# Optimization experiments

Measured on AMD Instinct MI355X. Metric: run time of the kernel, lower is better.

The kernel has to match this reference:

```python
import jax, jax.numpy as jnp
import numpy as np

# Dims: B=batch, C=n_car, N=n_node, E=embed_dim, H=n_heads
B, C, N, E = 64, 8, 512, 512
H = 8
CLIP = 10.0


def setup_inputs() -> dict:
    key = jax.random.key(0)
    ks = jax.random.split(key, 12)
    s = 1.0 / np.sqrt(E)
    mask = jax.random.bernoulli(ks[10], 0.3, (B, C, 1, N))
    mask = mask.at[..., 0].set(False)  # ensure at least one unmasked node per (b,c)
    return {
        "node_embeddings": jax.random.normal(ks[0], (B, N, E), jnp.float32),
        "graph_embedding": jax.random.normal(ks[1], (B, E), jnp.float32),
        "step_context": jax.random.normal(ks[2], (B, C, 1, E + 2), jnp.float32),
        "mask": mask,
        "Wk1": jax.random.normal(ks[3], (E, E), jnp.float32) * s,
        "Wv": jax.random.normal(ks[4], (E, E), jnp.float32) * s,
        "Wk2": jax.random.normal(ks[5], (E, E), jnp.float32) * s,
        "Wq_fixed": jax.random.normal(ks[6], (E, E), jnp.float32) * s,
        "Wout": jax.random.normal(ks[7], (E, E), jnp.float32) * s,
        "Wq_step": jax.random.normal(ks[8], (E, E + 2), jnp.float32) * s,
        "v": jax.random.uniform(ks[9], (E,), jnp.float32, -s, s),
    }


def reference(node_embeddings, graph_embedding, step_context, mask,
              Wk1, Wv, Wk2, Wq_fixed, Wout, Wq_step, v):
    dh = E // H
    neg = jnp.asarray(-1e9, node_embeddings.dtype)

    # compute_static: projections (torch Linear: x @ W.T). K/V/Q_fixed are
    # broadcast over the car dim instead of materialized via .repeat (same math).
    Q_fixed = (graph_embedding @ Wq_fixed.T)[:, None, None, :]  # [B,1,1,E]
    K1 = node_embeddings @ Wk1.T                                 # [B,N,E]
    V = node_embeddings @ Wv.T                                   # [B,N,E]
    K2 = node_embeddings @ Wk2.T                                 # [B,N,E]

    # compute_dynamic
    Q_step = step_context @ Wq_step.T                            # [B,C,1,E]
    Q1 = Q_fixed + Q_step                                        # [B,C,1,E]

    # MHA (need_W=False): split heads, masked scaled dot-product, merge heads.
    qh = Q1.reshape(B, C, H, dh)                                 # q-len 1 squeezed
    kh = K1.reshape(B, N, H, dh)
    vh = V.reshape(B, N, H, dh)
    scores = jnp.einsum('bchd,bnhd->bchn', qh, kh) * (1.0 / np.sqrt(dh))
    m = mask[:, :, 0, :][:, :, None, :]                          # [B,C,1,N]
    scores = jnp.where(m, neg, scores)
    attn = jax.nn.softmax(scores, axis=-1)
    heads = jnp.einsum('bchn,bnhd->bchd', attn, vh).reshape(B, C, E)
    Q3 = heads @ Wout.T                                          # [B,C,E] (Q2.squeeze(2))

    # Pointer logits (SHA): u = tanh(Q_fixed+Q_step) @ v, repeated over E,
    # dotted with K2 => u_scalar * sum_e K2, then tanh-clipped and masked.
    u_scalar = jnp.einsum('bcqe,e->bcq', jnp.tanh(Q1), v)        # [B,C,1]
    k2sum = K2.sum(-1)                                           # [B,N]
    raw = u_scalar * k2sum[:, None, :]                           # [B,C,N]
    logits = CLIP * jnp.tanh(raw * (1.0 / np.sqrt(E)))
    logits = jnp.where(mask[:, :, 0, :], neg, logits)
    logits = logits.reshape(B, C * N)                            # view(batch, -1)
    return logits, Q3
```

## Files before the change

kernel.cpp:

```cpp
#include <hip/hip_runtime.h>


typedef _Float16 f16x8 __attribute__((ext_vector_type(8)));
typedef _Float16 f16x2 __attribute__((ext_vector_type(2)));
typedef float f32x4 __attribute__((ext_vector_type(4)));

__device__ __forceinline__ void async16(const void* g, void* l) {
  __builtin_amdgcn_global_load_lds(
      (const __attribute__((address_space(1))) unsigned int*)g,
      (__attribute__((address_space(3))) unsigned int*)l, 16, 0, 0);
}

__global__ __launch_bounds__(256) void prep_w(const float* __restrict__ Wk1,
                                              const float* __restrict__ Wv,
                                              const float* __restrict__ Wk2,
                                              _Float16* __restrict__ W1h,
                                              _Float16* __restrict__ W2h,
                                              float* __restrict__ colsum) {
  const int bid = blockIdx.x;
  if (bid < 16) {
    const int tx = threadIdx.x & 31, ty = threadIdx.x >> 5;
    const int col = bid * 32 + tx;
    float s = 0.f;
#pragma unroll 4
    for (int e = ty * 64; e < ty * 64 + 64; ++e) s += Wk2[e * 512 + col];
    __shared__ float red[8][32];
    red[ty][tx] = s;
    __syncthreads();
    if (ty == 0) {
      float t = 0.f;
#pragma unroll
      for (int g = 0; g < 8; ++g) t += red[g][tx];
      colsum[col] = t;
    }
  } else {
    const int cb = bid - 16;
    const float* src = (cb < 128) ? Wk1 : Wv;
    _Float16* dst = (cb < 128) ? W1h : W2h;
    const size_t off = (size_t)(cb & 127) * 2048 + threadIdx.x * 8;
    float4 a = *(const float4*)(src + off);
    float4 b = *(const float4*)(src + off + 4);
    union { _Float16 h[8]; uint4 u; } pk;
    pk.h[0] = (_Float16)a.x; pk.h[1] = (_Float16)a.y;
    pk.h[2] = (_Float16)a.z; pk.h[3] = (_Float16)a.w;
    pk.h[4] = (_Float16)b.x; pk.h[5] = (_Float16)b.y;
    pk.h[6] = (_Float16)b.z; pk.h[7] = (_Float16)b.w;
    *(uint4*)(dst + off) = pk.u;
  }
}

__global__ __launch_bounds__(256) void k2sum_kernel(const float* __restrict__ ne,
                                                    const float* __restrict__ colsum,
                                                    float* __restrict__ k2sum) {
  const int wave = threadIdx.x >> 6, lane = threadIdx.x & 63;
  const int row = blockIdx.x * 4 + wave;
  float s = 0.f;
#pragma unroll
  for (int i = 0; i < 8; ++i) {
    int k = i * 64 + lane;
    s += ne[(size_t)row * 512 + k] * colsum[k];
  }
#pragma unroll
  for (int off = 32; off; off >>= 1) s += __shfl_down(s, off, 64);
  if (lane == 0) k2sum[row] = s;
}

__global__ __launch_bounds__(256) void q1_mfma_kernel(
    const float* __restrict__ ge, const float* __restrict__ sc,
    const float* __restrict__ Wqf, const float* __restrict__ Wqs,
    float* __restrict__ Q1) {
  const int mb = blockIdx.x, nb = blockIdx.y, ks = blockIdx.z;
  const int tid = threadIdx.x;
  const int lane = tid & 63, wave = tid >> 6;
  const int wm = (wave >> 1) * 32, wn = (wave & 1) * 32;

  __shared__ __align__(16) _Float16 As[64][40];
  __shared__ __align__(16) _Float16 Ws[64][40];

  f32x4 acc[2][2] = {};
  const int qd = (lane >> 4) * 8, rr = lane & 15;

  for (int kt = 0; kt < 9; ++kt) {
    const int kb = ks * 288 + kt * 32;
#pragma unroll
    for (int f0 = 0; f0 < 2; ++f0) {
      int f = tid + f0 * 256;
      int r = f >> 3, c4 = (f & 7) * 4;
      int m = mb * 64 + r;
      int e = nb * 64 + r;
#pragma unroll
      for (int j = 0; j < 4; ++j) {
        int k = kb + c4 + j;
        float a = 0.f, w = 0.f;
        if (k < 512) {
          a = ge[(m >> 3) * 512 + k];
          w = Wqf[(size_t)e * 512 + k];
        } else if (k < 1026) {
          a = sc[(size_t)m * 514 + (k - 512)];
          w = Wqs[(size_t)e * 514 + (k - 512)];
        }
        As[r][c4 + j] = (_Float16)a;
        Ws[r][c4 + j] = (_Float16)w;
      }
    }
    __syncthreads();
    f16x8 af[2], bfr[2];
#pragma unroll
    for (int mi = 0; mi < 2; ++mi) af[mi] = *(const f16x8*)&As[wm + mi * 16 + rr][qd];
#pragma unroll
    for (int ni = 0; ni < 2; ++ni) bfr[ni] = *(const f16x8*)&Ws[wn + ni * 16 + rr][qd];
#pragma unroll
    for (int mi = 0; mi < 2; ++mi)
#pragma unroll
      for (int ni = 0; ni < 2; ++ni)
        acc[mi][ni] =
            __builtin_amdgcn_mfma_f32_16x16x32_f16(af[mi], bfr[ni], acc[mi][ni], 0, 0, 0);
    __syncthreads();
  }

  const int col = lane & 15, rq = (lane >> 4) * 4;
#pragma unroll
  for (int mi = 0; mi < 2; ++mi)
#pragma unroll
    for (int ni = 0; ni < 2; ++ni)
#pragma unroll
      for (int r = 0; r < 4; ++r) {
        int m = mb * 64 + wm + mi * 16 + rq + r;
        int e = nb * 64 + wn + ni * 16 + col;
        atomicAdd(&Q1[(size_t)m * 512 + e], acc[mi][ni][r]);
      }
}

__global__ __launch_bounds__(256, 2) void gemm_kv(
    const float* __restrict__ A, const _Float16* __restrict__ W1,
    const _Float16* __restrict__ W2, _Float16* __restrict__ K1,
    _Float16* __restrict__ V) {
  const int nb = blockIdx.x;
  const int mb = blockIdx.y;
  const int tid = threadIdx.x, lane = tid & 63, wave = tid >> 6;
  const int wm = (wave >> 1) * 64, wn = (wave & 1) * 64;
  const int row0 = mb * 128, col0 = nb * 128;

  __shared__ __align__(16) _Float16 As[128][72];
  __shared__ __align__(16) _Float16 W1s[128 * 64];
  __shared__ __align__(16) _Float16 W2s[128 * 64];

  f32x4 acc1[4][4] = {}, acc2[4][4] = {};
  const int qd = (lane >> 4) * 8, rr = lane & 15;
  const int wlr = lane >> 3, wlc = lane & 7;

  for (int kt = 0; kt < 8; ++kt) {
    const int kbase = kt * 64;
#pragma unroll
    for (int j = 0; j < 4; ++j) {
      int r = wave * 32 + j * 8 + wlr;
      int c = wlc ^ (r & 7);
      size_t goff = (size_t)(col0 + r) * 512 + kbase + c * 8;
      async16(W1 + goff, &W1s[(wave * 32 + j * 8) * 64]);
      async16(W2 + goff, &W2s[(wave * 32 + j * 8) * 64]);
    }
#pragma unroll
    for (int i = 0; i < 4; ++i) {
      int f = tid + i * 256;
      int r = f >> 3, c8 = (f & 7) * 8;
      const float* ap = A + (size_t)(row0 + r) * 512 + kbase + c8;
      float4 a0 = *(const float4*)ap;
      float4 a1 = *(const float4*)(ap + 4);
      union { _Float16 h[8]; uint4 u; } pk;
      pk.h[0] = (_Float16)a0.x; pk.h[1] = (_Float16)a0.y;
      pk.h[2] = (_Float16)a0.z; pk.h[3] = (_Float16)a0.w;
      pk.h[4] = (_Float16)a1.x; pk.h[5] = (_Float16)a1.y;
      pk.h[6] = (_Float16)a1.z; pk.h[7] = (_Float16)a1.w;
      *(uint4*)&As[r][c8] = pk.u;
    }
    __syncthreads();
#pragma unroll
    for (int k0 = 0; k0 < 64; k0 += 32) {
      const int q = (k0 >> 3) + (lane >> 4);
      f16x8 af[4], b1[4], b2[4];
#pragma unroll
      for (int mi = 0; mi < 4; ++mi)
        af[mi] = *(const f16x8*)&As[wm + mi * 16 + rr][k0 + qd];
#pragma unroll
      for (int ni = 0; ni < 4; ++ni) {
        int rw = wn + ni * 16 + rr;
        int slot = q ^ (rw & 7);
        b1[ni] = *(const f16x8*)&W1s[rw * 64 + slot * 8];
        b2[ni] = *(const f16x8*)&W2s[rw * 64 + slot * 8];
      }
#pragma unroll
      for (int mi = 0; mi < 4; ++mi)
#pragma unroll
        for (int ni = 0; ni < 4; ++ni) {
          acc1[mi][ni] =
              __builtin_amdgcn_mfma_f32_16x16x32_f16(af[mi], b1[ni], acc1[mi][ni], 0, 0, 0);
          acc2[mi][ni] =
              __builtin_amdgcn_mfma_f32_16x16x32_f16(af[mi], b2[ni], acc2[mi][ni], 0, 0, 0);
        }
    }
    __syncthreads();
  }

  const int col = lane & 15, rq = (lane >> 4) * 4;
#pragma unroll
  for (int mi = 0; mi < 4; ++mi)
#pragma unroll
    for (int ni = 0; ni < 4; ++ni)
#pragma unroll
      for (int r = 0; r < 4; ++r) {
        size_t m = row0 + wm + mi * 16 + rq + r;
        size_t e = col0 + wn + ni * 16 + col;
        K1[m * 512 + e] = (_Float16)acc1[mi][ni][r];
        V[m * 512 + e] = (_Float16)acc2[mi][ni][r];
      }
}

__global__ __launch_bounds__(256) void attn_kernel(
    const float* __restrict__ Q1, const _Float16* __restrict__ K1,
    const _Float16* __restrict__ V, const int* __restrict__ mask,
    float* __restrict__ heads) {
  const int bid = blockIdx.x;
  const int b = bid & 63, c = bid >> 6;
  const int bc = b * 8 + c;
  const int tid = threadIdx.x;
  const int wave = tid >> 6, lane = tid & 63;
  const int m = lane & 15, q = lane >> 4;

  __shared__ float att[8][512];
  __shared__ __align__(16) _Float16 kt[64 * 512];

  f16x8 aflo = {}, afhi = {};
  if (m < 8) {
    const float* qp = Q1 + (size_t)bc * 512 + m * 64 + q * 8;
    float4 l0 = *(const float4*)qp, l1 = *(const float4*)(qp + 4);
    float4 h0 = *(const float4*)(qp + 32), h1 = *(const float4*)(qp + 36);
    aflo[0] = (_Float16)l0.x; aflo[1] = (_Float16)l0.y;
    aflo[2] = (_Float16)l0.z; aflo[3] = (_Float16)l0.w;
    aflo[4] = (_Float16)l1.x; aflo[5] = (_Float16)l1.y;
    aflo[6] = (_Float16)l1.z; aflo[7] = (_Float16)l1.w;
    afhi[0] = (_Float16)h0.x; afhi[1] = (_Float16)h0.y;
    afhi[2] = (_Float16)h0.z; afhi[3] = (_Float16)h0.w;
    afhi[4] = (_Float16)h1.x; afhi[5] = (_Float16)h1.y;
    afhi[6] = (_Float16)h1.z; afhi[7] = (_Float16)h1.w;
  }
  f16x8 afr[16];
#pragma unroll
  for (int s = 0; s < 16; ++s) {
    f16x8 z = {};
    afr[s] = (s == 2 * m) ? aflo : ((s == 2 * m + 1) ? afhi : z);
  }

  const _Float16* Kb = K1 + (size_t)b * 262144;
  for (int t = 0; t < 8; ++t) {
#pragma unroll
    for (int j = 0; j < 16; ++j) {
      int n = wave * 16 + j;
      int cg = (lane & 0x38) | ((lane ^ n) & 7);
      async16(Kb + (size_t)(t * 64 + n) * 512 + cg * 8, &kt[n * 512]);
    }
    __syncthreads();
    const int nl = wave * 16 + m;
    f32x4 acc = {};
#pragma unroll
    for (int s = 0; s < 16; ++s) {
      int cc = s * 4 + q;
      int slot = (cc & 0x38) | ((cc ^ nl) & 7);
      f16x8 bf = *(const f16x8*)&kt[nl * 512 + slot * 8];
      acc = __builtin_amdgcn_mfma_f32_16x16x32_f16(afr[s], bf, acc, 0, 0, 0);
    }
#pragma unroll
    for (int r = 0; r < 4; ++r) {
      int h = q * 4 + r;
      if (h < 8) att[h][t * 64 + wave * 16 + m] = acc[r];
    }
    __syncthreads();
  }

  for (int hh = wave; hh < 8; hh += 4) {
    float sv[8];
    float mx = -3e38f;
#pragma unroll
    for (int i = 0; i < 8; ++i) {
      int n = i * 64 + lane;
      float x = mask[(size_t)bc * 512 + n] ? -1e9f : att[hh][n] * 0.125f;
      sv[i] = x;
      mx = fmaxf(mx, x);
    }
#pragma unroll
    for (int off = 32; off; off >>= 1) mx = fmaxf(mx, __shfl_xor(mx, off, 64));
    float sum = 0.f;
#pragma unroll
    for (int i = 0; i < 8; ++i) {
      sv[i] = __expf(sv[i] - mx);
      sum += sv[i];
    }
#pragma unroll
    for (int off = 32; off; off >>= 1) sum += __shfl_xor(sum, off, 64);
    float inv = 1.f / sum;
#pragma unroll
    for (int i = 0; i < 8; ++i) att[hh][i * 64 + lane] = sv[i] * inv;
  }
  __syncthreads();

  const int e0 = tid * 2;
  const int he = e0 >> 6;
  float a0 = 0.f, a1 = 0.f;
  const _Float16* Vb = V + (size_t)b * 262144;
  for (int t = 0; t < 16; ++t) {
#pragma unroll
    for (int i = 0; i < 8; ++i) {
      int n = wave * 8 + i;
      async16(Vb + (size_t)(t * 32 + n) * 512 + lane * 8, &kt[n * 512]);
    }
    __syncthreads();
#pragma unroll
    for (int n = 0; n < 32; ++n) {
      float at = att[he][t * 32 + n];
      f16x2 hv = *(const f16x2*)&kt[n * 512 + e0];
      a0 += at * (float)hv[0];
      a1 += at * (float)hv[1];
    }
    __syncthreads();
  }
  heads[(size_t)bc * 512 + e0] = a0;
  heads[(size_t)bc * 512 + e0 + 1] = a1;
}

__global__ __launch_bounds__(256) void gemm_out64(const float* __restrict__ A,
                                                  const float* __restrict__ W,
                                                  float* __restrict__ C) {
  const int mb = blockIdx.x, nb = blockIdx.y, ks = blockIdx.z;
  const int tid = threadIdx.x;
  const int lane = tid & 63, wave = tid >> 6;
  const int wm = (wave >> 1) * 32, wn = (wave & 1) * 32;

  __shared__ __align__(16) _Float16 As[64][40];
  __shared__ __align__(16) _Float16 Ws[64][40];

  f32x4 acc[2][2] = {};
  const int qd = (lane >> 4) * 8, rr = lane & 15;

  for (int kt = 0; kt < 8; ++kt) {
    const int kb = ks * 256 + kt * 32;
#pragma unroll
    for (int f0 = 0; f0 < 2; ++f0) {
      int f = tid + f0 * 256;
      int r = f >> 3, c4 = (f & 7) * 4;
      float4 a = *(const float4*)(A + (size_t)(mb * 64 + r) * 512 + kb + c4);
      float4 w = *(const float4*)(W + (size_t)(nb * 64 + r) * 512 + kb + c4);
      As[r][c4 + 0] = (_Float16)a.x; As[r][c4 + 1] = (_Float16)a.y;
      As[r][c4 + 2] = (_Float16)a.z; As[r][c4 + 3] = (_Float16)a.w;
      Ws[r][c4 + 0] = (_Float16)w.x; Ws[r][c4 + 1] = (_Float16)w.y;
      Ws[r][c4 + 2] = (_Float16)w.z; Ws[r][c4 + 3] = (_Float16)w.w;
    }
    __syncthreads();
    f16x8 af[2], bfr[2];
#pragma unroll
    for (int mi = 0; mi < 2; ++mi) af[mi] = *(const f16x8*)&As[wm + mi * 16 + rr][qd];
#pragma unroll
    for (int ni = 0; ni < 2; ++ni) bfr[ni] = *(const f16x8*)&Ws[wn + ni * 16 + rr][qd];
#pragma unroll
    for (int mi = 0; mi < 2; ++mi)
#pragma unroll
      for (int ni = 0; ni < 2; ++ni)
        acc[mi][ni] =
            __builtin_amdgcn_mfma_f32_16x16x32_f16(af[mi], bfr[ni], acc[mi][ni], 0, 0, 0);
    __syncthreads();
  }

  const int col = lane & 15, rq = (lane >> 4) * 4;
#pragma unroll
  for (int mi = 0; mi < 2; ++mi)
#pragma unroll
    for (int ni = 0; ni < 2; ++ni)
#pragma unroll
      for (int r = 0; r < 4; ++r) {
        int m = mb * 64 + wm + mi * 16 + rq + r;
        int e = nb * 64 + wn + ni * 16 + col;
        atomicAdd(&C[(size_t)m * 512 + e], acc[mi][ni][r]);
      }
}

__global__ __launch_bounds__(256) void logits_u_kernel(
    const float* __restrict__ Q1, const float* __restrict__ v,
    const float* __restrict__ k2s, const int* __restrict__ mask,
    float* __restrict__ out) {
  const int bc = blockIdx.x;
  const int b = bc >> 3;
  const int tid = threadIdx.x;
  const int wave = tid >> 6, lane = tid & 63;

  float p = tanhf(Q1[(size_t)bc * 512 + tid]) * v[tid] +
            tanhf(Q1[(size_t)bc * 512 + tid + 256]) * v[tid + 256];
#pragma unroll
  for (int off = 32; off; off >>= 1) p += __shfl_down(p, off, 64);
  __shared__ float red[4];
  __shared__ float su;
  if (lane == 0) red[wave] = p;
  __syncthreads();
  if (tid == 0) su = red[0] + red[1] + red[2] + red[3];
  __syncthreads();
  const float u = su;

#pragma unroll
  for (int i = 0; i < 2; ++i) {
    int n = tid + i * 256;
    int idx = bc * 512 + n;
    out[idx] = mask[idx] ? -1e9f
                         : 10.f * tanhf(u * k2s[b * 512 + n] * 0.04419417382415922f);
  }
}

extern "C" void kernel_launch(void* const* d_in, const int* in_sizes, int n_in,
                              void* d_out, int out_size, void* d_ws, size_t ws_size,
                              hipStream_t stream) {
  const float* ne = (const float*)d_in[0];
  const float* ge = (const float*)d_in[1];
  const float* sc = (const float*)d_in[2];
  const int* mask = (const int*)d_in[3];
  const float* Wk1 = (const float*)d_in[4];
  const float* Wv = (const float*)d_in[5];
  const float* Wk2 = (const float*)d_in[6];
  const float* Wqf = (const float*)d_in[7];
  const float* Wout = (const float*)d_in[8];
  const float* Wqs = (const float*)d_in[9];
  const float* v = (const float*)d_in[10];

  float* logits = (float*)d_out;
  float* q3 = (float*)d_out + 262144;

  char* ws = (char*)d_ws;
  _Float16* K1 = (_Float16*)(ws + 0);
  _Float16* V = (_Float16*)(ws + 33554432);
  float* Q1 = (float*)(ws + 67108864);
  float* heads = (float*)(ws + 68157440);
  float* k2sum = (float*)(ws + 69206016);
  float* colsum = (float*)(ws + 69337088);
  _Float16* W1h = (_Float16*)(ws + 69339136);
  _Float16* W2h = (_Float16*)(ws + 69863424);

  hipMemsetAsync(Q1, 0, 1048576, stream);
  hipMemsetAsync(q3, 0, 1048576, stream);
  prep_w<<<272, 256, 0, stream>>>(Wk1, Wv, Wk2, W1h, W2h, colsum);
  q1_mfma_kernel<<<dim3(8, 8, 4), 256, 0, stream>>>(ge, sc, Wqf, Wqs, Q1);
  gemm_kv<<<dim3(4, 256), 256, 0, stream>>>(ne, W1h, W2h, K1, V);
  k2sum_kernel<<<8192, 256, 0, stream>>>(ne, colsum, k2sum);
  attn_kernel<<<512, 256, 0, stream>>>(Q1, K1, V, mask, heads);
  gemm_out64<<<dim3(8, 8, 2), 256, 0, stream>>>(heads, Wout, q3);
  logits_u_kernel<<<512, 256, 0, stream>>>(Q1, v, k2sum, mask, logits);
}
```

Measured before the change: 251.3 us.

## Fuse k2sum into KV GEMM, store V transposed, restructure attention per (batch, head)

The k2sum reduction now happens inside the KV projection GEMM, which reuses the fp32 node-embedding tiles it already loads, so the separate kernel that re-read node_embeddings is removed. V is written transposed through an LDS staging buffer, and the grid is remapped so blocks sharing a batch run on the same XCD. Attention now runs one block per (batch, head) and covers all 8 cars at once, using MFMA for both QK and PV instead of scalar FMA loops. This cuts redundant K/V reads across cars, but adds atomics on k2sum, an extra memset, and divergent nb==0 work inside the GEMM.

Result: slower. 271.6 us (+8.1%).

```diff
diff --git a/kernel.cpp b/kernel.cpp
--- a/kernel.cpp
+++ b/kernel.cpp
@@ -2,7 +2,6 @@
 
 
 typedef _Float16 f16x8 __attribute__((ext_vector_type(8)));
-typedef _Float16 f16x2 __attribute__((ext_vector_type(2)));
 typedef float f32x4 __attribute__((ext_vector_type(4)));
 
 __device__ __forceinline__ void async16(const void* g, void* l) {
@@ -49,22 +48,6 @@
   }
 }
 
-__global__ __launch_bounds__(256) void k2sum_kernel(const float* __restrict__ ne,
-                                                    const float* __restrict__ colsum,
-                                                    float* __restrict__ k2sum) {
-  const int wave = threadIdx.x >> 6, lane = threadIdx.x & 63;
-  const int row = blockIdx.x * 4 + wave;
-  float s = 0.f;
-#pragma unroll
-  for (int i = 0; i < 8; ++i) {
-    int k = i * 64 + lane;
-    s += ne[(size_t)row * 512 + k] * colsum[k];
-  }
-#pragma unroll
-  for (int off = 32; off; off >>= 1) s += __shfl_down(s, off, 64);
-  if (lane == 0) k2sum[row] = s;
-}
-
 __global__ __launch_bounds__(256) void q1_mfma_kernel(
     const float* __restrict__ ge, const float* __restrict__ sc,
     const float* __restrict__ Wqf, const float* __restrict__ Wqs,
@@ -133,19 +116,22 @@
 
 __global__ __launch_bounds__(256, 2) void gemm_kv(
     const float* __restrict__ A, const _Float16* __restrict__ W1,
-    const _Float16* __restrict__ W2, _Float16* __restrict__ K1,
-    _Float16* __restrict__ V) {
-  const int nb = blockIdx.x;
-  const int mb = blockIdx.y;
+    const _Float16* __restrict__ W2, const float* __restrict__ colsum,
+    _Float16* __restrict__ K1, _Float16* __restrict__ Vt,
+    float* __restrict__ k2sum) {
+  const int bid = blockIdx.x;
+  const int xcd = bid & 7, ii = bid >> 3;
+  const int nb = ii & 3, mb = xcd * 32 + (ii >> 2);
   const int tid = threadIdx.x, lane = tid & 63, wave = tid >> 6;
   const int wm = (wave >> 1) * 64, wn = (wave & 1) * 64;
   const int row0 = mb * 128, col0 = nb * 128;
+  const int b = mb >> 2;
 
   __shared__ __align__(16) _Float16 As[128][72];
-  __shared__ __align__(16) _Float16 W1s[128 * 64];
-  __shared__ __align__(16) _Float16 W2s[128 * 64];
+  __shared__ __align__(16) _Float16 Wbuf[2][128 * 64];
 
   f32x4 acc1[4][4] = {}, acc2[4][4] = {};
+  float k2p[4] = {};
   const int qd = (lane >> 4) * 8, rr = lane & 15;
   const int wlr = lane >> 3, wlc = lane & 7;
 
@@ -156,8 +142,8 @@
       int r = wave * 32 + j * 8 + wlr;
       int c = wlc ^ (r & 7);
       size_t goff = (size_t)(col0 + r) * 512 + kbase + c * 8;
-      async16(W1 + goff, &W1s[(wave * 32 + j * 8) * 64]);
-      async16(W2 + goff, &W2s[(wave * 32 + j * 8) * 64]);
+      async16(W1 + goff, &Wbuf[0][(wave * 32 + j * 8) * 64]);
+      async16(W2 + goff, &Wbuf[1][(wave * 32 + j * 8) * 64]);
     }
 #pragma unroll
     for (int i = 0; i < 4; ++i) {
@@ -172,6 +158,13 @@
       pk.h[4] = (_Float16)a1.x; pk.h[5] = (_Float16)a1.y;
       pk.h[6] = (_Float16)a1.z; pk.h[7] = (_Float16)a1.w;
       *(uint4*)&As[r][c8] = pk.u;
+      if (nb == 0) {
+        const float* cp = colsum + kbase + c8;
+        float4 c0 = *(const float4*)cp;
+        float4 c1 = *(const float4*)(cp + 4);
+        k2p[i] += a0.x * c0.x + a0.y * c0.y + a0.z * c0.z + a0.w * c0.w +
+                  a1.x * c1.x + a1.y * c1.y + a1.z * c1.z + a1.w * c1.w;
+      }
     }
     __syncthreads();
 #pragma unroll
@@ -185,8 +178,8 @@
       for (int ni = 0; ni < 4; ++ni) {
         int rw = wn + ni * 16 + rr;
         int slot = q ^ (rw & 7);
-        b1[ni] = *(const f16x8*)&W1s[rw * 64 + slot * 8];
-        b2[ni] = *(const f16x8*)&W2s[rw * 64 + slot * 8];
+        b1[ni] = *(const f16x8*)&Wbuf[0][rw * 64 + slot * 8];
+        b2[ni] = *(const f16x8*)&Wbuf[1][rw * 64 + slot * 8];
       }
 #pragma unroll
       for (int mi = 0; mi < 4; ++mi)
@@ -201,6 +194,14 @@
     __syncthreads();
   }
 
+  if (nb == 0) {
+#pragma unroll
+    for (int i = 0; i < 4; ++i) {
+      int r = (tid + i * 256) >> 3;
+      atomicAdd(&k2sum[row0 + r], k2p[i]);
+    }
+  }
+
   const int col = lane & 15, rq = (lane >> 4) * 4;
 #pragma unroll
   for (int mi = 0; mi < 4; ++mi)
@@ -211,119 +212,168 @@
         size_t m = row0 + wm + mi * 16 + rq + r;
         size_t e = col0 + wn + ni * 16 + col;
         K1[m * 512 + e] = (_Float16)acc1[mi][ni][r];
-        V[m * 512 + e] = (_Float16)acc2[mi][ni][r];
-      }
+      }
+
+  _Float16* Vts = &Wbuf[0][0];
+#pragma unroll
+  for (int mi = 0; mi < 4; ++mi)
+#pragma unroll
+    for (int ni = 0; ni < 4; ++ni) {
+      int n0 = wm + mi * 16 + rq;
+      int el = wn + ni * 16 + col;
+      int cn = n0 >> 3, half = (n0 >> 2) & 1;
+      int slot = cn ^ (el & 7);
+      union { _Float16 h[4]; unsigned long long u; } pk;
+#pragma unroll
+      for (int r = 0; r < 4; ++r) pk.h[r] = (_Float16)acc2[mi][ni][r];
+      *(unsigned long long*)&Vts[el * 128 + slot * 8 + half * 4] = pk.u;
+    }
+  __syncthreads();
+  const int nbase = row0 & 511;
+#pragma unroll
+  for (int i = 0; i < 8; ++i) {
+    int f = tid + i * 256;
+    int el = f >> 4, c16 = f & 15;
+    int slot = c16 ^ (el & 7);
+    uint4 val = *(const uint4*)&Vts[el * 128 + slot * 8];
+    *(uint4*)(Vt + (size_t)b * 262144 + (size_t)(col0 + el) * 512 + nbase + c16 * 8) = val;
+  }
 }
 
 __global__ __launch_bounds__(256) void attn_kernel(
     const float* __restrict__ Q1, const _Float16* __restrict__ K1,
-    const _Float16* __restrict__ V, const int* __restrict__ mask,
+    const _Float16* __restrict__ Vt, const int* __restrict__ mask,
     float* __restrict__ heads) {
   const int bid = blockIdx.x;
-  const int b = bid & 63, c = bid >> 6;
-  const int bc = b * 8 + c;
-  const int tid = threadIdx.x;
-  const int wave = tid >> 6, lane = tid & 63;
-  const int m = lane & 15, q = lane >> 4;
-
-  __shared__ float att[8][512];
-  __shared__ __align__(16) _Float16 kt[64 * 512];
-
-  f16x8 aflo = {}, afhi = {};
-  if (m < 8) {
-    const float* qp = Q1 + (size_t)bc * 512 + m * 64 + q * 8;
-    float4 l0 = *(const float4*)qp, l1 = *(const float4*)(qp + 4);
-    float4 h0 = *(const float4*)(qp + 32), h1 = *(const float4*)(qp + 36);
-    aflo[0] = (_Float16)l0.x; aflo[1] = (_Float16)l0.y;
-    aflo[2] = (_Float16)l0.z; aflo[3] = (_Float16)l0.w;
-    aflo[4] = (_Float16)l1.x; aflo[5] = (_Float16)l1.y;
-    aflo[6] = (_Float16)l1.z; aflo[7] = (_Float16)l1.w;
-    afhi[0] = (_Float16)h0.x; afhi[1] = (_Float16)h0.y;
-    afhi[2] = (_Float16)h0.z; afhi[3] = (_Float16)h0.w;
-    afhi[4] = (_Float16)h1.x; afhi[5] = (_Float16)h1.y;
-    afhi[6] = (_Float16)h1.z; afhi[7] = (_Float16)h1.w;
-  }
-  f16x8 afr[16];
-#pragma unroll
-  for (int s = 0; s < 16; ++s) {
-    f16x8 z = {};
-    afr[s] = (s == 2 * m) ? aflo : ((s == 2 * m + 1) ? afhi : z);
-  }
-
-  const _Float16* Kb = K1 + (size_t)b * 262144;
-  for (int t = 0; t < 8; ++t) {
-#pragma unroll
-    for (int j = 0; j < 16; ++j) {
-      int n = wave * 16 + j;
-      int cg = (lane & 0x38) | ((lane ^ n) & 7);
-      async16(Kb + (size_t)(t * 64 + n) * 512 + cg * 8, &kt[n * 512]);
-    }
-    __syncthreads();
-    const int nl = wave * 16 + m;
-    f32x4 acc = {};
-#pragma unroll
-    for (int s = 0; s < 16; ++s) {
-      int cc = s * 4 + q;
-      int slot = (cc & 0x38) | ((cc ^ nl) & 7);
-      f16x8 bf = *(const f16x8*)&kt[nl * 512 + slot * 8];
-      acc = __builtin_amdgcn_mfma_f32_16x16x32_f16(afr[s], bf, acc, 0, 0, 0);
-    }
+  const int b = bid >> 3, h = bid & 7;
+  const int tid = threadIdx.x, wave = tid >> 6, lane = tid & 63;
+  const int q = lane >> 4, cl = lane & 15;
+
+  __shared__ __align__(16) _Float16 kt[256 * 64];
+  __shared__ __align__(16) _Float16 P[16][520];
+  __shared__ float red[4][8];
+
+  f16x8 af[2];
+  {
+    const float* qp = Q1 + (size_t)(b * 8 + (cl & 7)) * 512 + h * 64 + q * 8;
+#pragma unroll
+    for (int s = 0; s < 2; ++s) {
+      float4 l0 = *(const float4*)(qp + s * 32);
+      float4 l1 = *(const float4*)(qp + s * 32 + 4);
+      af[s][0] = (_Float16)l0.x; af[s][1] = (_Float16)l0.y;
+      af[s][2] = (_Float16)l0.z; af[s][3] = (_Float16)l0.w;
+      af[s][4] = (_Float16)l1.x; af[s][5] = (_Float16)l1.y;
+      af[s][6] = (_Float16)l1.z; af[s][7] = (_Float16)l1.w;
+    }
+  }
+
+  f32x4 acc[8] = {};
+  const _Float16* Kb = K1 + (size_t)b * 262144 + h * 64;
+  for (int h2 = 0; h2 < 2; ++h2) {
+#pragma unroll
+    for (int j = 0; j < 8; ++j) {
+      int r = wave * 64 + j * 8 + (lane >> 3);
+      int cg = (lane & 7) ^ (r & 7);
+      async16(Kb + (size_t)(h2 * 256 + r) * 512 + cg * 8, &kt[(wave * 64 + j * 8) * 64]);
+    }
+    __syncthreads();
+#pragma unroll
+    for (int tt = 0; tt < 4; ++tt) {
+      int rn = wave * 64 + tt * 16 + cl;
+#pragma unroll
+      for (int s = 0; s < 2; ++s) {
+        int slot = (s * 4 + q) ^ (cl & 7);
+        f16x8 bf = *(const f16x8*)&kt[rn * 64 + slot * 8];
+        acc[h2 * 4 + tt] =
+            __builtin_amdgcn_mfma_f32_16x16x32_f16(af[s], bf, acc[h2 * 4 + tt], 0, 0, 0);
+      }
+    }
+    __syncthreads();
+  }
+
+  float gmax[4], rsum[4];
+  if (q < 2) {
+    float mx[4] = {-3e38f, -3e38f, -3e38f, -3e38f};
+#pragma unroll
+    for (int t = 0; t < 8; ++t) {
+      int n = (t >> 2) * 256 + wave * 64 + (t & 3) * 16 + cl;
+#pragma unroll
+      for (int r = 0; r < 4; ++r) {
+        int c = q * 4 + r;
+        float x = mask[(size_t)(b * 8 + c) * 512 + n] ? -1e9f : acc[t][r] * 0.125f;
+        acc[t][r] = x;
+        mx[r] = fmaxf(mx[r], x);
+      }
+    }
+#pragma unroll
+    for (int off = 1; off < 16; off <<= 1)
+#pragma unroll
+      for (int r = 0; r < 4; ++r) mx[r] = fmaxf(mx[r], __shfl_xor(mx[r], off, 64));
+    if (cl == 0)
+#pragma unroll
+      for (int r = 0; r < 4; ++r) red[wave][q * 4 + r] = mx[r];
+  }
+  __syncthreads();
+  if (q < 2) {
 #pragma unroll
     for (int r = 0; r < 4; ++r) {
-      int h = q * 4 + r;
-      if (h < 8) att[h][t * 64 + wave * 16 + m] = acc[r];
-    }
-    __syncthreads();
-  }
-
-  for (int hh = wave; hh < 8; hh += 4) {
-    float sv[8];
-    float mx = -3e38f;
-#pragma unroll
-    for (int i = 0; i < 8; ++i) {
-      int n = i * 64 + lane;
-      float x = mask[(size_t)bc * 512 + n] ? -1e9f : att[hh][n] * 0.125f;
-      sv[i] = x;
-      mx = fmaxf(mx, x);
-    }
-#pragma unroll
-    for (int off = 32; off; off >>= 1) mx = fmaxf(mx, __shfl_xor(mx, off, 64));
-    float sum = 0.f;
-#pragma unroll
-    for (int i = 0; i < 8; ++i) {
-      sv[i] = __expf(sv[i] - mx);
-      sum += sv[i];
-    }
-#pragma unroll
-    for (int off = 32; off; off >>= 1) sum += __shfl_xor(sum, off, 64);
-    float inv = 1.f / sum;
-#pragma unroll
-    for (int i = 0; i < 8; ++i) att[hh][i * 64 + lane] = sv[i] * inv;
+      int c = q * 4 + r;
+      gmax[r] = fmaxf(fmaxf(red[0][c], red[1][c]), fmaxf(red[2][c], red[3][c]));
+    }
   }
   __syncthreads();
-
-  const int e0 = tid * 2;
-  const int he = e0 >> 6;
-  float a0 = 0.f, a1 = 0.f;
-  const _Float16* Vb = V + (size_t)b * 262144;
-  for (int t = 0; t < 16; ++t) {
-#pragma unroll
-    for (int i = 0; i < 8; ++i) {
-      int n = wave * 8 + i;
-      async16(Vb + (size_t)(t * 32 + n) * 512 + lane * 8, &kt[n * 512]);
-    }
-    __syncthreads();
-#pragma unroll
-    for (int n = 0; n < 32; ++n) {
-      float at = att[he][t * 32 + n];
-      f16x2 hv = *(const f16x2*)&kt[n * 512 + e0];
-      a0 += at * (float)hv[0];
-      a1 += at * (float)hv[1];
-    }
-    __syncthreads();
-  }
-  heads[(size_t)bc * 512 + e0] = a0;
-  heads[(size_t)bc * 512 + e0 + 1] = a1;
+  if (q < 2) {
+#pragma unroll
+    for (int r = 0; r < 4; ++r) rsum[r] = 0.f;
+#pragma unroll
+    for (int t = 0; t < 8; ++t) {
+      int n = (t >> 2) * 256 + wave * 64 + (t & 3) * 16 + cl;
+#pragma unroll
+      for (int r = 0; r < 4; ++r) {
+        float e = __expf(acc[t][r] - gmax[r]);
+        rsum[r] += e;
+        P[q * 4 + r][n] = (_Float16)e;
+      }
+    }
+#pragma unroll
+    for (int off = 1; off < 16; off <<= 1)
+#pragma unroll
+      for (int r = 0; r < 4; ++r) rsum[r] += __shfl_xor(rsum[r], off, 64);
+    if (cl == 0)
+#pragma unroll
+      for (int r = 0; r < 4; ++r) red[wave][q * 4 + r] = rsum[r];
+  }
+  __syncthreads();
+
+  f32x4 pacc = {};
+  const _Float16* Vb = Vt + (size_t)b * 262144 + (size_t)h * 64 * 512;
+  for (int h2 = 0; h2 < 2; ++h2) {
+#pragma unroll
+    for (int j = 0; j < 8; ++j) {
+      int r = wave * 16 + j * 2 + (lane >> 5);
+      int cg = (lane & 31) ^ (r & 7);
+      async16(Vb + (size_t)r * 512 + h2 * 256 + cg * 8, &kt[(wave * 16 + j * 2) * 256]);
+    }
+    __syncthreads();
+    int rn = wave * 16 + cl;
+#pragma unroll
+    for (int sl = 0; sl < 8; ++sl) {
+      int slot = (sl * 4 + q) ^ (cl & 7);
+      f16x8 bf = *(const f16x8*)&kt[rn * 256 + slot * 8];
+      f16x8 pa = *(const f16x8*)&P[cl][h2 * 256 + sl * 32 + q * 8];
+      pacc = __builtin_amdgcn_mfma_f32_16x16x32_f16(pa, bf, pacc, 0, 0, 0);
+    }
+    __syncthreads();
+  }
+
+  if (q < 2) {
+#pragma unroll
+    for (int r = 0; r < 4; ++r) {
+      int c = q * 4 + r;
+      float inv = 1.f / (red[0][c] + red[1][c] + red[2][c] + red[3][c]);
+      heads[(size_t)(b * 8 + c) * 512 + h * 64 + wave * 16 + cl] = pacc[r] * inv;
+    }
+  }
 }
 
 __global__ __launch_bounds__(256) void gemm_out64(const float* __restrict__ A,
@@ -431,7 +481,7 @@
 
   char* ws = (char*)d_ws;
   _Float16* K1 = (_Float16*)(ws + 0);
-  _Float16* V = (_Float16*)(ws + 33554432);
+  _Float16* Vt = (_Float16*)(ws + 33554432);
   float* Q1 = (float*)(ws + 67108864);
   float* heads = (float*)(ws + 68157440);
   float* k2sum = (float*)(ws + 69206016);
@@ -441,11 +491,11 @@
 
   hipMemsetAsync(Q1, 0, 1048576, stream);
   hipMemsetAsync(q3, 0, 1048576, stream);
+  hipMemsetAsync(k2sum, 0, 131072, stream);
   prep_w<<<272, 256, 0, stream>>>(Wk1, Wv, Wk2, W1h, W2h, colsum);
   q1_mfma_kernel<<<dim3(8, 8, 4), 256, 0, stream>>>(ge, sc, Wqf, Wqs, Q1);
-  gemm_kv<<<dim3(4, 256), 256, 0, stream>>>(ne, W1h, W2h, K1, V);
-  k2sum_kernel<<<8192, 256, 0, stream>>>(ne, colsum, k2sum);
-  attn_kernel<<<512, 256, 0, stream>>>(Q1, K1, V, mask, heads);
+  gemm_kv<<<1024, 256, 0, stream>>>(ne, W1h, W2h, colsum, K1, Vt, k2sum);
+  attn_kernel<<<512, 256, 0, stream>>>(Q1, K1, Vt, mask, heads);
   gemm_out64<<<dim3(8, 8, 2), 256, 0, stream>>>(heads, Wout, q3);
   logits_u_kernel<<<512, 256, 0, stream>>>(Q1, v, k2sum, mask, logits);
 }
```
